# Optimization experiments

Measured on AMD Instinct MI355X. Metric: run time of the kernel, lower is better.

## Reference

```python
import jax, jax.numpy as jnp
import numpy as np

N_WIRES = 8
EMBED = 768
B, S = 16, 2048


def setup_inputs() -> dict:
    key = jax.random.key(0)
    k1, k2, k3, k4 = jax.random.split(key, 4)
    return {
        "x": jax.random.normal(k1, (B, S, EMBED), dtype=jnp.float32),
        "w_q": jax.random.normal(k2, (N_WIRES, EMBED), dtype=jnp.float32) * (1.0 / np.sqrt(EMBED)),
        "w_out": jax.random.normal(k3, (EMBED, N_WIRES), dtype=jnp.float32) * (1.0 / np.sqrt(N_WIRES)),
        "q_params": jax.random.normal(k4, (N_WIRES,), dtype=jnp.float32),
    }


def _simulate(angles):
    """Statevector sim: RX(angle_w) on each wire w, then ring of CNOTs, then <Z_w>.
    angles: [B, S, n].  Returns [B, S, n] Pauli-Z expectations."""
    b, s, n = angles.shape
    # |0...0> initial state, one qubit per trailing axis of size 2
    state = jnp.zeros((b, s) + (2,) * n, dtype=jnp.complex64)
    state = state.at[(slice(None), slice(None)) + (0,) * n].set(1.0)
    # RX gates (data angle + learned angle already fused in `angles`)
    for w in range(n):
        ax = 2 + w
        half = angles[..., w] * 0.5
        bshape = (b, s) + (1,) * (n - 1)
        c = jnp.cos(half).reshape(bshape)
        si = jnp.sin(half).reshape(bshape)
        a0 = jnp.take(state, 0, axis=ax)
        a1 = jnp.take(state, 1, axis=ax)
        state = jnp.stack([c * a0 - 1j * si * a1, -1j * si * a0 + c * a1], axis=ax)
    # CNOT chain: (0,1),(1,2),...,(n-2,n-1),(n-1,0)
    for src, tgt in [(i, i + 1) for i in range(n - 1)] + [(n - 1, 0)]:
        sax, tax = 2 + src, 2 + tgt
        a0 = jnp.take(state, 0, axis=sax)
        a1 = jnp.take(state, 1, axis=sax)
        tadj = tax - (1 if tax > sax else 0)  # target axis after removing src axis
        state = jnp.stack([a0, jnp.flip(a1, axis=tadj)], axis=sax)
    probs = jnp.real(state * jnp.conj(state))  # [B,S,2,...,2]
    zs = []
    for w in range(n):
        axes = tuple(a for a in range(2, 2 + n) if a != 2 + w)
        marg = probs.sum(axis=axes)  # [B,S,2]
        zs.append(marg[..., 0] - marg[..., 1])
    return jnp.stack(zs, axis=-1)


def reference(x, w_q, w_out, q_params):
    # per-token RX angles; two RX on same wire commute -> fuse data + learned angle
    angles = jnp.einsum("bse,ne->bsn", x, w_q) + q_params  # [B,S,n]
    z = _simulate(angles)  # [B,S,n]
    return jnp.einsum("bsn,en->bse", z, w_out)  # [B,S,E]
```

## Files before the change

### kernel.cpp

```cpp
#include <hip/hip_runtime.h>
#include <math.h>


using f32x4 = __attribute__((ext_vector_type(4))) float;

constexpr int E  = 768;
constexpr int NW = 8;
constexpr int BLOCK = 256;
constexpr int TOKENS = 16 * 2048;
constexpr int TOK_PER_WAVE  = 4;
constexpr int TOK_PER_BLOCK = TOK_PER_WAVE * 4;
constexpr int GRID = TOKENS / TOK_PER_BLOCK;

__device__ __forceinline__ float dot12(const f32x4& a0, const f32x4& a1, const f32x4& a2,
                                       const f32x4& b0, const f32x4& b1, const f32x4& b2) {
    return a0.x*b0.x + a0.y*b0.y + a0.z*b0.z + a0.w*b0.w
         + a1.x*b1.x + a1.y*b1.y + a1.z*b1.z + a1.w*b1.w
         + a2.x*b2.x + a2.y*b2.y + a2.z*b2.z + a2.w*b2.w;
}

__device__ __forceinline__ void circuit8(const float zf[NW], int lane, float qpl,
                                         float z[NW]) {
    float v4[4];
    #pragma unroll
    for (int i = 0; i < 4; ++i) {
        float a = zf[2*i], b = zf[2*i+1];
        float keep = (lane & 1) ? b : a;
        float send = (lane & 1) ? a : b;
        v4[i] = keep + __shfl_xor(send, 1, 64);
    }
    float v2[2];
    #pragma unroll
    for (int i = 0; i < 2; ++i) {
        float a = v4[2*i], b = v4[2*i+1];
        float keep = (lane & 2) ? b : a;
        float send = (lane & 2) ? a : b;
        v2[i] = keep + __shfl_xor(send, 2, 64);
    }
    float a = v2[0], b = v2[1];
    float keep = (lane & 4) ? b : a;
    float send = (lane & 4) ? a : b;
    float v = keep + __shfl_xor(send, 4, 64);
    v += __shfl_xor(v, 8, 64);
    v += __shfl_xor(v, 16, 64);
    v += __shfl_xor(v, 32, 64);
    float c = __cosf(v + qpl);
    float cx = __shfl_xor(c, 1, 64);
    float e0 = (lane & 1) ? cx : c;
    float e1 = (lane & 1) ? c : cx;
    float e0x = __shfl_xor(e0, 2, 64), e1x = __shfl_xor(e1, 2, 64);
    float f0 = (lane & 2) ? e0x : e0;
    float f1 = (lane & 2) ? e1x : e1;
    float f2 = (lane & 2) ? e0  : e0x;
    float f3 = (lane & 2) ? e1  : e1x;
    float f0x = __shfl_xor(f0, 4, 64), f1x = __shfl_xor(f1, 4, 64);
    float f2x = __shfl_xor(f2, 4, 64), f3x = __shfl_xor(f3, 4, 64);
    float c0 = (lane & 4) ? f0x : f0;
    float c1 = (lane & 4) ? f1x : f1;
    float c2 = (lane & 4) ? f2x : f2;
    float c3 = (lane & 4) ? f3x : f3;
    float c4 = (lane & 4) ? f0  : f0x;
    float c5 = (lane & 4) ? f1  : f1x;
    float c6 = (lane & 4) ? f2  : f2x;
    float c7 = (lane & 4) ? f3  : f3x;
    float p1 = c0*c1, p2 = p1*c2, p3 = p2*c3, p4 = p3*c4;
    float p5 = p4*c5, p6 = p5*c6, p7 = p6*c7;
    float s  = c1*c2*c3*c4*c5*c6*c7;
    z[0] = s;  z[1] = p1; z[2] = p2; z[3] = p3;
    z[4] = p4; z[5] = p5; z[6] = p6; z[7] = p7;
}

__global__ __launch_bounds__(BLOCK, 4)
void mhaq_kernel(const float* __restrict__ x,
                 const float* __restrict__ w_q,
                 const float* __restrict__ w_out,
                 const float* __restrict__ q_params,
                 float* __restrict__ out)
{
    __shared__ float wq_lds[NW][E];
    __shared__ float wt_lds[NW][E];

    const int tid  = threadIdx.x;
    const int wave = tid >> 6;
    const int lane = tid & 63;
    const int col  = lane * 4;
    const int t0   = blockIdx.x * TOK_PER_BLOCK + wave * TOK_PER_WAVE;

    f32x4 xv[TOK_PER_WAVE][3];
    #pragma unroll
    for (int tt = 0; tt < TOK_PER_WAVE; ++tt) {
        const f32x4* xp = reinterpret_cast<const f32x4*>(x + (size_t)(t0 + tt) * E);
        #pragma unroll
        for (int k = 0; k < 3; ++k)
            xv[tt][k] = xp[lane + k * 64];
    }

    {
        const f32x4* src = reinterpret_cast<const f32x4*>(w_q);
        f32x4* dst = reinterpret_cast<f32x4*>(&wq_lds[0][0]);
        #pragma unroll
        for (int r = 0; r < (NW * E / 4) / BLOCK; ++r)
            dst[tid + r * BLOCK] = src[tid + r * BLOCK];
    }
    {
        const f32x4* src = reinterpret_cast<const f32x4*>(w_out);
        #pragma unroll
        for (int r = 0; r < (NW * E / 4) / BLOCK; ++r) {
            int idx = tid + r * BLOCK;
            f32x4 v = src[idx];
            int e  = idx >> 1;
            int n0 = (idx & 1) * 4;
            wt_lds[n0 + 0][e] = v.x;
            wt_lds[n0 + 1][e] = v.y;
            wt_lds[n0 + 2][e] = v.z;
            wt_lds[n0 + 3][e] = v.w;
        }
    }
    const float qpl = q_params[lane & 7];
    __syncthreads();

    float zf[TOK_PER_WAVE][NW];
    #pragma unroll
    for (int n = 0; n < NW; ++n) {
        const f32x4 w0 = *reinterpret_cast<const f32x4*>(&wq_lds[n][col]);
        const f32x4 w1 = *reinterpret_cast<const f32x4*>(&wq_lds[n][col + 256]);
        const f32x4 w2 = *reinterpret_cast<const f32x4*>(&wq_lds[n][col + 512]);
        #pragma unroll
        for (int tt = 0; tt < TOK_PER_WAVE; ++tt)
            zf[tt][n] = dot12(xv[tt][0], xv[tt][1], xv[tt][2], w0, w1, w2);
    }

    float z[TOK_PER_WAVE][NW];
    #pragma unroll
    for (int tt = 0; tt < TOK_PER_WAVE; ++tt)
        circuit8(zf[tt], lane, qpl, z[tt]);

    #pragma unroll
    for (int k = 0; k < 3; ++k) {
        const int e0 = k * 256 + col;
        f32x4 wv[NW];
        #pragma unroll
        for (int n = 0; n < NW; ++n)
            wv[n] = *reinterpret_cast<const f32x4*>(&wt_lds[n][e0]);
        #pragma unroll
        for (int tt = 0; tt < TOK_PER_WAVE; ++tt) {
            float ox = 0.f, oy = 0.f, oz = 0.f, ow = 0.f;
            #pragma unroll
            for (int n = 0; n < NW; ++n) {
                ox += z[tt][n] * wv[n].x;
                oy += z[tt][n] * wv[n].y;
                oz += z[tt][n] * wv[n].z;
                ow += z[tt][n] * wv[n].w;
            }
            f32x4 o; o.x = ox; o.y = oy; o.z = oz; o.w = ow;
            *reinterpret_cast<f32x4*>(out + (size_t)(t0 + tt) * E + e0) = o;
        }
    }
}

extern "C" void kernel_launch(void* const* d_in, const int* in_sizes, int n_in,
                              void* d_out, int out_size, void* d_ws, size_t ws_size,
                              hipStream_t stream) {
    const float* x        = (const float*)d_in[0];
    const float* w_q      = (const float*)d_in[1];
    const float* w_out    = (const float*)d_in[2];
    const float* q_params = (const float*)d_in[3];
    float* out = (float*)d_out;

    hipLaunchKernelGGL(mhaq_kernel, dim3(GRID), dim3(BLOCK), 0, stream,
                       x, w_q, w_out, q_params, out);
}
```

Baseline: 36.36 us.

## Split fused kernel into z-compute and output-expand kernels via workspace

Splits the single fused kernel into two launches. The first computes the per-token 8-wire expectations and writes them to a workspace buffer. The second reads those values with scalar loads and expands them to 768 outputs using w_out. The aim is to separate the read-heavy and write-heavy phases so each kernel has a smaller LDS footprint and can reach higher occupancy. The cost is an extra launch and a small workspace round trip, and the original fused kernel is kept as a fallback when the workspace is too small.

```diff
diff --git a/kernel.cpp b/kernel.cpp
--- a/kernel.cpp
+++ b/kernel.cpp
@@ -71,14 +71,12 @@
 }
 
 __global__ __launch_bounds__(BLOCK, 4)
-void mhaq_kernel(const float* __restrict__ x,
-                 const float* __restrict__ w_q,
-                 const float* __restrict__ w_out,
-                 const float* __restrict__ q_params,
-                 float* __restrict__ out)
+void zcalc_kernel(const float* __restrict__ x,
+                  const float* __restrict__ w_q,
+                  const float* __restrict__ q_params,
+                  float* __restrict__ zout)
 {
     __shared__ float wq_lds[NW][E];
-    __shared__ float wt_lds[NW][E];
 
     const int tid  = threadIdx.x;
     const int wave = tid >> 6;
@@ -94,7 +92,6 @@
         for (int k = 0; k < 3; ++k)
             xv[tt][k] = xp[lane + k * 64];
     }
-
     {
         const f32x4* src = reinterpret_cast<const f32x4*>(w_q);
         f32x4* dst = reinterpret_cast<f32x4*>(&wq_lds[0][0]);
@@ -102,6 +99,54 @@
         for (int r = 0; r < (NW * E / 4) / BLOCK; ++r)
             dst[tid + r * BLOCK] = src[tid + r * BLOCK];
     }
+    const float qpl = q_params[lane & 7];
+    __syncthreads();
+
+    float zf[TOK_PER_WAVE][NW];
+    #pragma unroll
+    for (int n = 0; n < NW; ++n) {
+        const f32x4 w0 = *reinterpret_cast<const f32x4*>(&wq_lds[n][col]);
+        const f32x4 w1 = *reinterpret_cast<const f32x4*>(&wq_lds[n][col + 256]);
+        const f32x4 w2 = *reinterpret_cast<const f32x4*>(&wq_lds[n][col + 512]);
+        #pragma unroll
+        for (int tt = 0; tt < TOK_PER_WAVE; ++tt)
+            zf[tt][n] = dot12(xv[tt][0], xv[tt][1], xv[tt][2], w0, w1, w2);
+    }
+
+    float z[TOK_PER_WAVE][NW];
+    #pragma unroll
+    for (int tt = 0; tt < TOK_PER_WAVE; ++tt)
+        circuit8(zf[tt], lane, qpl, z[tt]);
+
+    float sel[NW];
+    #pragma unroll
+    for (int n = 0; n < NW; ++n) {
+        float s01 = (lane & 8)  ? z[1][n] : z[0][n];
+        float s23 = (lane & 8)  ? z[3][n] : z[2][n];
+        sel[n]    = (lane & 16) ? s23 : s01;
+    }
+    float v01 = (lane & 1) ? sel[1] : sel[0];
+    float v23 = (lane & 1) ? sel[3] : sel[2];
+    float v45 = (lane & 1) ? sel[5] : sel[4];
+    float v67 = (lane & 1) ? sel[7] : sel[6];
+    float v03 = (lane & 2) ? v23 : v01;
+    float v47 = (lane & 2) ? v67 : v45;
+    float vv  = (lane & 4) ? v47 : v03;
+    if (lane < 32) zout[(size_t)t0 * NW + lane] = vv;
+}
+
+__global__ __launch_bounds__(BLOCK, 4)
+void expand_kernel(const float* __restrict__ z,
+                   const float* __restrict__ w_out,
+                   float* __restrict__ out)
+{
+    __shared__ float wt_lds[NW][E];
+
+    const int tid  = threadIdx.x;
+    const int wave = tid >> 6;
+    const int lane = tid & 63;
+    const int col  = lane * 4;
+
     {
         const f32x4* src = reinterpret_cast<const f32x4*>(w_out);
         #pragma unroll
@@ -116,6 +161,87 @@
             wt_lds[n0 + 3][e] = v.w;
         }
     }
+    __syncthreads();
+
+    const int t0u = __builtin_amdgcn_readfirstlane(
+        blockIdx.x * TOK_PER_BLOCK + wave * TOK_PER_WAVE);
+
+    float zz[TOK_PER_WAVE][NW];
+    #pragma unroll
+    for (int tt = 0; tt < TOK_PER_WAVE; ++tt) {
+        #pragma unroll
+        for (int n = 0; n < NW; ++n)
+            zz[tt][n] = z[(size_t)(t0u + tt) * NW + n];
+    }
+
+    #pragma unroll
+    for (int k = 0; k < 3; ++k) {
+        const int e0 = k * 256 + col;
+        f32x4 wv[NW];
+        #pragma unroll
+        for (int n = 0; n < NW; ++n)
+            wv[n] = *reinterpret_cast<const f32x4*>(&wt_lds[n][e0]);
+        #pragma unroll
+        for (int tt = 0; tt < TOK_PER_WAVE; ++tt) {
+            float ox = 0.f, oy = 0.f, oz = 0.f, ow = 0.f;
+            #pragma unroll
+            for (int n = 0; n < NW; ++n) {
+                ox += zz[tt][n] * wv[n].x;
+                oy += zz[tt][n] * wv[n].y;
+                oz += zz[tt][n] * wv[n].z;
+                ow += zz[tt][n] * wv[n].w;
+            }
+            f32x4 o; o.x = ox; o.y = oy; o.z = oz; o.w = ow;
+            *reinterpret_cast<f32x4*>(out + (size_t)(t0u + tt) * E + e0) = o;
+        }
+    }
+}
+
+__global__ __launch_bounds__(BLOCK, 4)
+void mhaq_fused(const float* __restrict__ x,
+                const float* __restrict__ w_q,
+                const float* __restrict__ w_out,
+                const float* __restrict__ q_params,
+                float* __restrict__ out)
+{
+    __shared__ float wq_lds[NW][E];
+    __shared__ float wt_lds[NW][E];
+
+    const int tid  = threadIdx.x;
+    const int wave = tid >> 6;
+    const int lane = tid & 63;
+    const int col  = lane * 4;
+    const int t0   = blockIdx.x * TOK_PER_BLOCK + wave * TOK_PER_WAVE;
+
+    f32x4 xv[TOK_PER_WAVE][3];
+    #pragma unroll
+    for (int tt = 0; tt < TOK_PER_WAVE; ++tt) {
+        const f32x4* xp = reinterpret_cast<const f32x4*>(x + (size_t)(t0 + tt) * E);
+        #pragma unroll
+        for (int k = 0; k < 3; ++k)
+            xv[tt][k] = xp[lane + k * 64];
+    }
+    {
+        const f32x4* src = reinterpret_cast<const f32x4*>(w_q);
+        f32x4* dst = reinterpret_cast<f32x4*>(&wq_lds[0][0]);
+        #pragma unroll
+        for (int r = 0; r < (NW * E / 4) / BLOCK; ++r)
+            dst[tid + r * BLOCK] = src[tid + r * BLOCK];
+    }
+    {
+        const f32x4* src = reinterpret_cast<const f32x4*>(w_out);
+        #pragma unroll
+        for (int r = 0; r < (NW * E / 4) / BLOCK; ++r) {
+            int idx = tid + r * BLOCK;
+            f32x4 v = src[idx];
+            int e  = idx >> 1;
+            int n0 = (idx & 1) * 4;
+            wt_lds[n0 + 0][e] = v.x;
+            wt_lds[n0 + 1][e] = v.y;
+            wt_lds[n0 + 2][e] = v.z;
+            wt_lds[n0 + 3][e] = v.w;
+        }
+    }
     const float qpl = q_params[lane & 7];
     __syncthreads();
 
@@ -129,7 +255,6 @@
         for (int tt = 0; tt < TOK_PER_WAVE; ++tt)
             zf[tt][n] = dot12(xv[tt][0], xv[tt][1], xv[tt][2], w0, w1, w2);
     }
-
     float z[TOK_PER_WAVE][NW];
     #pragma unroll
     for (int tt = 0; tt < TOK_PER_WAVE; ++tt)
@@ -167,6 +292,15 @@
     const float* q_params = (const float*)d_in[3];
     float* out = (float*)d_out;
 
-    hipLaunchKernelGGL(mhaq_kernel, dim3(GRID), dim3(BLOCK), 0, stream,
-                       x, w_q, w_out, q_params, out);
-}
+    const size_t z_bytes = (size_t)TOKENS * NW * sizeof(float);
+    if (ws_size >= z_bytes) {
+        float* z = (float*)d_ws;
+        hipLaunchKernelGGL(zcalc_kernel,  dim3(GRID), dim3(BLOCK), 0, stream,
+                           x, w_q, q_params, z);
+        hipLaunchKernelGGL(expand_kernel, dim3(GRID), dim3(BLOCK), 0, stream,
+                           z, w_out, out);
+    } else {
+        hipLaunchKernelGGL(mhaq_fused, dim3(GRID), dim3(BLOCK), 0, stream,
+                           x, w_q, w_out, q_params, out);
+    }
+}
```

Result: slower. 52.47 us (+44.3%).
